# Kernel optimization log

Measured on AMD Instinct MI355X. Metric: run time of the kernel, lower is better.

## Reference

```python
import jax, jax.numpy as jnp
import numpy as np

N_HEAD = 8
HEAD_DIM = 64
DIM = 512
INNER = N_HEAD * HEAD_DIM
ATT_THRESHOLD = 1e-4
SCALE = HEAD_DIM ** -0.5


def setup_inputs() -> dict:
    key = jax.random.key(0)
    ks = jax.random.split(key, 7)
    b, n, dn = 2, 2048, 2048
    fr = jax.random.normal(ks[0], (b, n, DIM), dtype=jnp.float32)
    dt = jax.random.normal(ks[1], (b, dn, DIM), dtype=jnp.float32)
    s = DIM ** -0.5
    Wq = jax.random.normal(ks[2], (DIM, INNER), dtype=jnp.float32) * s
    Wk = jax.random.normal(ks[3], (DIM, INNER), dtype=jnp.float32) * s
    Wv = jax.random.normal(ks[4], (DIM, INNER), dtype=jnp.float32) * s
    Wo = jax.random.normal(ks[5], (INNER, DIM), dtype=jnp.float32) * (INNER ** -0.5)
    bo = jax.random.normal(ks[6], (DIM,), dtype=jnp.float32) * 0.01
    return {"fr": fr, "dt": dt, "Wq": Wq, "Wk": Wk, "Wv": Wv, "Wo": Wo, "bo": bo}


def reference(fr, dt, Wq, Wk, Wv, Wo, bo):
    b, n, _ = fr.shape
    dn = dt.shape[1]
    # projections -> [b, seq, n_head, head_dim]
    q = (fr @ Wq).reshape(b, n, N_HEAD, HEAD_DIM)
    k = (dt @ Wk).reshape(b, dn, N_HEAD, HEAD_DIM)
    v = (dt @ Wv).reshape(b, dn, N_HEAD, HEAD_DIM)
    # full attention matrix [b, h, n, dn]
    scores = jnp.einsum('bihd,bjhd->bhij', q, k) * SCALE
    attn = jax.nn.softmax(scores, axis=-1)
    # torch .clip(t) with one positional arg clamps the MIN: max(attn, t)
    attn = jnp.maximum(attn, ATT_THRESHOLD) - ATT_THRESHOLD
    attn = attn / jnp.sum(attn, axis=-1, keepdims=True)
    out = jnp.einsum('bhij,bjhd->bihd', attn, v).reshape(b, n, INNER)
    return out @ Wo + bo
```

## Files before the change

kernel.cpp:

```cpp
#include <hip/hip_runtime.h>
#include <hip/hip_bf16.h>

#define BB 2
#define SEQ 2048
#define NHEAD 8
#define HD 64
#define ATT_T 1e-4f
#define QSCALE 0.18033688011112042f

typedef short s16x8 __attribute__((ext_vector_type(8)));
typedef float f32x16 __attribute__((ext_vector_type(16)));

#define MFMA32(a, b, c) __builtin_amdgcn_mfma_f32_32x32x16_bf16((a), (b), (c), 0, 0, 0)
#define EXP2(x) __builtin_amdgcn_exp2f(x)
#define SB0() __builtin_amdgcn_sched_barrier(0)
#define WAITVM0() __builtin_amdgcn_s_waitcnt(0x0F70)
#define WAITVM4() __builtin_amdgcn_s_waitcnt(0x0F74)
#define WAITVM8() __builtin_amdgcn_s_waitcnt(0x0F78)

__device__ __forceinline__ unsigned short bfr(float x) {
  __hip_bfloat16 h = __float2bfloat16(x);
  return __builtin_bit_cast(unsigned short, h);
}
__device__ __forceinline__ unsigned int packbf(float a, float b) {
  return (unsigned int)bfr(a) | ((unsigned int)bfr(b) << 16);
}
__device__ __forceinline__ unsigned int permpack(float a, float b) {
  return __builtin_amdgcn_perm(__builtin_bit_cast(unsigned int, b),
                               __builtin_bit_cast(unsigned int, a), 0x07060302u);
}
__device__ __forceinline__ void async16(const void* g, void* l) {
  __builtin_amdgcn_global_load_lds(
      (const __attribute__((address_space(1))) unsigned int*)g,
      (__attribute__((address_space(3))) unsigned int*)l, 16, 0, 0);
}

__global__ __launch_bounds__(256) void convT(const float* __restrict__ w0,
                                             const float* __restrict__ w1,
                                             const float* __restrict__ w2,
                                             const float* __restrict__ w3,
                                             unsigned short* __restrict__ o0,
                                             unsigned short* __restrict__ o1,
                                             unsigned short* __restrict__ o2,
                                             unsigned short* __restrict__ o3) {
  __shared__ float tle[64][65];
  const float* W = blockIdx.z == 0 ? w0 : blockIdx.z == 1 ? w1 : blockIdx.z == 2 ? w2 : w3;
  unsigned short* WT = blockIdx.z == 0 ? o0 : blockIdx.z == 1 ? o1 : blockIdx.z == 2 ? o2 : o3;
  const int r0 = blockIdx.y * 64, c0 = blockIdx.x * 64;
  const int tr = threadIdx.x >> 4;
  const int tc = threadIdx.x & 15;
  #pragma unroll
  for (int i = 0; i < 4; i++) {
    int r = tr + i * 16;
    float4 v = *(const float4*)(W + (size_t)(r0 + r) * 512 + c0 + tc * 4);
    tle[r][tc * 4 + 0] = v.x;
    tle[r][tc * 4 + 1] = v.y;
    tle[r][tc * 4 + 2] = v.z;
    tle[r][tc * 4 + 3] = v.w;
  }
  __syncthreads();
  #pragma unroll
  for (int i = 0; i < 4; i++) {
    int c = tr + i * 16;
    int rr = tc * 4;
    uint2 p;
    p.x = packbf(tle[rr + 0][c], tle[rr + 1][c]);
    p.y = packbf(tle[rr + 2][c], tle[rr + 3][c]);
    *(uint2*)(WT + (size_t)(c0 + c) * 512 + r0 + rr) = p;
  }
}

__global__ __launch_bounds__(256) void gemm_qkv(const float* __restrict__ frF,
                                                const float* __restrict__ dtF,
                                                const unsigned short* __restrict__ WqT,
                                                const unsigned short* __restrict__ WkT,
                                                const unsigned short* __restrict__ WvT,
                                                unsigned short* __restrict__ Qp,
                                                unsigned short* __restrict__ Kp,
                                                unsigned short* __restrict__ VTp) {
  __shared__ __align__(16) unsigned short smem[24576];
  unsigned short* Asm = smem;
  unsigned short* Bsm = smem + 8192;
  const int tid = threadIdx.x, lane = tid & 63, w = tid >> 6;
  const int l31 = lane & 31, lh = lane >> 5;
  const int m0 = blockIdx.y * 64, n0 = blockIdx.x * 128;
  const int z = blockIdx.z;
  const float* A = z == 0 ? frF : dtF;
  const unsigned short* BT = z == 0 ? WqT : (z == 1 ? WkT : WvT);
  unsigned short* OP = z == 0 ? Qp : (z == 1 ? Kp : VTp);
  const float scale = z == 0 ? QSCALE : 1.0f;

  const int arow = tid >> 2, aseg = tid & 3;
  const float* Ap = A + (size_t)(m0 + arow) * 512 + aseg * 16;
  const int aoff = (arow >> 5) * 2048 + aseg * 512 + (arow & 31) * 8;

  auto stageB = [&](int kt, int buf) {
    const int k0 = kt * 64;
    #pragma unroll
    for (int i = 0; i < 4; i++) {
      int r = w * 4 + i, gn = r >> 2, ks = r & 3;
      async16(BT + (size_t)(n0 + gn * 32 + l31) * 512 + k0 + ks * 16 + lh * 8,
              Bsm + buf * 8192 + r * 512);
    }
  };
  auto ldA = [&](int kt, float4* r4) {
    #pragma unroll
    for (int i = 0; i < 4; i++) r4[i] = *(const float4*)(Ap + kt * 64 + i * 4);
  };
  auto wrA = [&](int buf, const float4* r4) {
    uint4 w0v, w1v;
    w0v.x = packbf(r4[0].x, r4[0].y); w0v.y = packbf(r4[0].z, r4[0].w);
    w0v.z = packbf(r4[1].x, r4[1].y); w0v.w = packbf(r4[1].z, r4[1].w);
    w1v.x = packbf(r4[2].x, r4[2].y); w1v.y = packbf(r4[2].z, r4[2].w);
    w1v.z = packbf(r4[3].x, r4[3].y); w1v.w = packbf(r4[3].z, r4[3].w);
    *(uint4*)(Asm + buf * 4096 + aoff) = w0v;
    *(uint4*)(Asm + buf * 4096 + aoff + 256) = w1v;
  };

  f32x16 acc[2];
  #pragma unroll
  for (int j = 0; j < 2; j++)
    #pragma unroll
    for (int r = 0; r < 16; r++) acc[j][r] = 0.f;

  float4 areg[4];
  ldA(0, areg);
  stageB(0, 0);
  wrA(0, areg);
  ldA(1, areg);

  for (int kt = 0; kt < 8; ++kt) {
    __syncthreads();
    if (kt + 1 < 8) {
      const int nb = (kt + 1) & 1;
      stageB(kt + 1, nb);
      wrA(nb, areg);
      if (kt + 2 < 8) ldA(kt + 2, areg);
    }
    const int buf = kt & 1;
    const unsigned short* as = Asm + buf * 4096 + (w & 1) * 2048;
    const unsigned short* bs = Bsm + buf * 8192 + (w >> 1) * 4096;
    #pragma unroll
    for (int ks = 0; ks < 4; ++ks) {
      s16x8 af = *(const s16x8*)(as + ks * 512 + lane * 8);
      s16x8 b0 = *(const s16x8*)(bs + ks * 512 + lane * 8);
      s16x8 b1 = *(const s16x8*)(bs + 2048 + ks * 512 + lane * 8);
      acc[0] = MFMA32(af, b0, acc[0]);
      acc[1] = MFMA32(af, b1, acc[1]);
    }
  }

  const int wm = (w & 1) * 32, wn = (w >> 1) * 64;
  const int bb = m0 >> 11, s0 = m0 & 2047;
  __syncthreads();
  if (z <= 1) {
    #pragma unroll
    for (int j = 0; j < 2; j++)
      #pragma unroll
      for (int r = 0; r < 16; r++) {
        int mm = wm + (r & 3) + 8 * (r >> 2) + 4 * lh;
        int nn = wn + j * 32 + l31;
        smem[mm * 136 + nn] = bfr(acc[j][r] * scale);
      }
    __syncthreads();
    #pragma unroll
    for (int it = 0; it < 4; ++it) {
      int c = tid + it * 256;
      int mm = c >> 4, seg = c & 15;
      uint4 vdat = *(const uint4*)(smem + mm * 136 + seg * 8);
      int n = n0 + seg * 8, h = n >> 6, d = n & 63;
      *(uint4*)(OP + ((size_t)((bb * NHEAD + h) * SEQ + s0 + mm)) * HD + d) = vdat;
    }
  } else {
    #pragma unroll
    for (int j = 0; j < 2; j++)
      #pragma unroll
      for (int r = 0; r < 16; r += 2) {
        int mm = wm + (r & 3) + 8 * (r >> 2) + 4 * lh;
        int nn = wn + j * 32 + l31;
        *(unsigned int*)(smem + nn * 72 + mm) = packbf(acc[j][r], acc[j][r + 1]);
      }
    __syncthreads();
    #pragma unroll
    for (int it = 0; it < 4; ++it) {
      int c = tid + it * 256;
      int nn = c >> 3, seg = c & 7;
      uint4 vdat = *(const uint4*)(smem + nn * 72 + seg * 8);
      int n = n0 + nn, h = n >> 6, d = n & 63;
      *(uint4*)(OP + ((size_t)((bb * NHEAD + h) * HD + d)) * SEQ + s0 + seg * 8) = vdat;
    }
  }
}

__global__ __launch_bounds__(256) void gemm_out(const unsigned short* __restrict__ A,
                                                const unsigned short* __restrict__ BT,
                                                const float* __restrict__ bias,
                                                float* __restrict__ O) {
  __shared__ __align__(16) unsigned short smem[16384];
  unsigned short* Asm = smem;
  unsigned short* Bsm = smem + 8192;
  const int tid = threadIdx.x, lane = tid & 63, w = tid >> 6;
  const int l31 = lane & 31, lh = lane >> 5;
  const int m0 = blockIdx.y * 64, n0 = blockIdx.x * 64;

  auto stage = [&](int kt, int buf) {
    const int k0 = kt * 64;
    #pragma unroll
    for (int i = 0; i < 2; i++) {
      int r = w * 2 + i, g = r >> 2, ks = r & 3;
      async16(A + (size_t)(m0 + g * 32 + l31) * 512 + k0 + ks * 16 + lh * 8,
              Asm + buf * 4096 + r * 512);
      async16(BT + (size_t)(n0 + g * 32 + l31) * 512 + k0 + ks * 16 + lh * 8,
              Bsm + buf * 4096 + r * 512);
    }
  };

  f32x16 acc;
  #pragma unroll
  for (int r = 0; r < 16; r++) acc[r] = 0.f;

  stage(0, 0);
  for (int kt = 0; kt < 8; ++kt) {
    __syncthreads();
    if (kt + 1 < 8) stage(kt + 1, (kt + 1) & 1);
    const int buf = kt & 1;
    const unsigned short* as = Asm + buf * 4096 + (w & 1) * 2048;
    const unsigned short* bs = Bsm + buf * 4096 + (w >> 1) * 2048;
    #pragma unroll
    for (int ks = 0; ks < 4; ++ks) {
      s16x8 af = *(const s16x8*)(as + ks * 512 + lane * 8);
      s16x8 bf = *(const s16x8*)(bs + ks * 512 + lane * 8);
      acc = MFMA32(af, bf, acc);
    }
  }

  const int wm = (w & 1) * 32, wn = (w >> 1) * 32;
  float bv = bias[n0 + wn + l31];
  #pragma unroll
  for (int r = 0; r < 16; r++) {
    int mm = wm + (r & 3) + 8 * (r >> 2) + 4 * lh;
    O[(size_t)(m0 + mm) * 512 + n0 + wn + l31] = acc[r] + bv;
  }
}

__global__ __launch_bounds__(256, 2) void attn_mfma(const unsigned short* __restrict__ Q,
                                                    const unsigned short* __restrict__ K,
                                                    const unsigned short* __restrict__ VT,
                                                    unsigned short* __restrict__ O) {
  __shared__ __align__(16) unsigned short arena[4][8192];
  __shared__ float larr[4][64];
  __shared__ float warr[4][64];

  const int tid = threadIdx.x;
  const int lane = tid & 63;
  const int w = tid >> 6;
  const int l31 = lane & 31, lh = lane >> 5;

  const int bid = blockIdx.x;
  const int g = bid & 7, j = bid >> 3;
  const int bh = g * 2 + (j >> 5);
  const int qt = j & 31;

  const unsigned short* Qh = Q + (size_t)bh * SEQ * HD;
  const unsigned short* Kh = K + (size_t)bh * SEQ * HD;
  const unsigned short* VTh = VT + (size_t)bh * HD * SEQ;

  s16x8 qf[2][4];
  #pragma unroll
  for (int q2 = 0; q2 < 2; q2++)
    #pragma unroll
    for (int t = 0; t < 4; t++)
      qf[q2][t] = *(const s16x8*)(Qh + (size_t)(qt * 64 + q2 * 32 + l31) * HD + 16 * t + 8 * lh);

  unsigned short* kbuf = &arena[w][0];
  unsigned short* vbuf = &arena[w][4096];
  const int kbase = w * 512;

  auto stageK = [&](int c, int slot) {
    const unsigned short* base = Kh + (size_t)(kbase + c * 32 + l31) * HD + lh * 8;
    #pragma unroll
    for (int tt = 0; tt < 4; tt++)
      async16(base + tt * 16, kbuf + slot * 2048 + tt * 512);
  };
  auto stageV = [&](int c, int slot) {
    #pragma unroll
    for (int dh = 0; dh < 2; dh++)
      #pragma unroll
      for (int kc = 0; kc < 2; kc++)
        async16(VTh + (size_t)(dh * 32 + l31) * SEQ + kbase + c * 32 + kc * 16 + lh * 8,
                vbuf + slot * 2048 + (dh * 2 + kc) * 512);
  };

  float lsum[2] = {0.f, 0.f};
  f32x16 scp[2];

  auto accum_l = [&]() {
    #pragma unroll
    for (int q2 = 0; q2 < 2; q2++) {
      float s0 = 0.f, s1 = 0.f, s2 = 0.f, s3 = 0.f;
      #pragma unroll
      for (int r = 0; r < 4; r++) {
        s0 += EXP2(scp[q2][r]);
        s1 += EXP2(scp[q2][4 + r]);
        s2 += EXP2(scp[q2][8 + r]);
        s3 += EXP2(scp[q2][12 + r]);
      }
      lsum[q2] += (s0 + s1) + (s2 + s3);
    }
  };

  stageK(0, 0);
  for (int c = 0; c < 16; ++c) {
    const int slot = c & 1;
    if (c + 1 < 16) stageK(c + 1, slot ^ 1);
    if (c > 0) accum_l();
    if (c + 1 < 16) { WAITVM4(); } else { WAITVM0(); }
    SB0();
    s16x8 kf[4];
    #pragma unroll
    for (int tt = 0; tt < 4; tt++)
      kf[tt] = *(const s16x8*)(kbuf + slot * 2048 + tt * 512 + lane * 8);
    #pragma unroll
    for (int q2 = 0; q2 < 2; q2++) {
      f32x16 sc;
      #pragma unroll
      for (int r = 0; r < 16; r++) sc[r] = 0.f;
      #pragma unroll
      for (int tt = 0; tt < 4; tt++) sc = MFMA32(kf[tt], qf[q2][tt], sc);
      scp[q2] = sc;
    }
  }
  accum_l();
  #pragma unroll
  for (int q2 = 0; q2 < 2; q2++) lsum[q2] += __shfl_xor(lsum[q2], 32);
  if (lh == 0) { larr[w][l31] = lsum[0]; larr[w][32 + l31] = lsum[1]; }
  __syncthreads();
  float tl[2];
  #pragma unroll
  for (int q2 = 0; q2 < 2; q2++)
    tl[q2] = ATT_T * (larr[0][q2 * 32 + l31] + larr[1][q2 * 32 + l31] +
                      larr[2][q2 * 32 + l31] + larr[3][q2 * 32 + l31]);

  f32x16 acc[2][2];
  #pragma unroll
  for (int q2 = 0; q2 < 2; q2++)
    #pragma unroll
    for (int dh = 0; dh < 2; dh++)
      #pragma unroll
      for (int r = 0; r < 16; r++) acc[q2][dh][r] = 0.f;
  float wacc[2] = {0.f, 0.f};
  s16x8 vfp[2][2];

  auto softmax_pv = [&]() {
    s16x8 pf[2][2];
    #pragma unroll
    for (int q2 = 0; q2 < 2; q2++) {
      uint2 quads[4];
      #pragma unroll
      for (int gq = 0; gq < 4; gq++) {
        float u0 = fmaxf(EXP2(scp[q2][4 * gq + 0]) - tl[q2], 0.f);
        float u1 = fmaxf(EXP2(scp[q2][4 * gq + 1]) - tl[q2], 0.f);
        float u2 = fmaxf(EXP2(scp[q2][4 * gq + 2]) - tl[q2], 0.f);
        float u3 = fmaxf(EXP2(scp[q2][4 * gq + 3]) - tl[q2], 0.f);
        wacc[q2] += (u0 + u1) + (u2 + u3);
        quads[gq].x = permpack(u0, u1);
        quads[gq].y = permpack(u2, u3);
      }
      #pragma unroll
      for (int tp = 0; tp < 2; tp++) {
        uint2 ea, eb;
        ea.x = (unsigned)__shfl_xor((int)quads[2 * tp].x, 32);
        ea.y = (unsigned)__shfl_xor((int)quads[2 * tp].y, 32);
        eb.x = (unsigned)__shfl_xor((int)quads[2 * tp + 1].x, 32);
        eb.y = (unsigned)__shfl_xor((int)quads[2 * tp + 1].y, 32);
        uint4 fr;
        if (lh == 0) { fr.x = quads[2 * tp].x; fr.y = quads[2 * tp].y; fr.z = ea.x; fr.w = ea.y; }
        else         { fr.x = eb.x; fr.y = eb.y; fr.z = quads[2 * tp + 1].x; fr.w = quads[2 * tp + 1].y; }
        pf[q2][tp] = __builtin_bit_cast(s16x8, fr);
      }
    }
    #pragma unroll
    for (int q2 = 0; q2 < 2; q2++)
      #pragma unroll
      for (int dh = 0; dh < 2; dh++) {
        acc[q2][dh] = MFMA32(pf[q2][0], vfp[dh][0], acc[q2][dh]);
        acc[q2][dh] = MFMA32(pf[q2][1], vfp[dh][1], acc[q2][dh]);
      }
  };

  stageK(0, 0);
  stageV(0, 0);
  for (int c = 0; c < 16; ++c) {
    const int slot = c & 1;
    if (c + 1 < 16) { stageK(c + 1, slot ^ 1); stageV(c + 1, slot ^ 1); }
    if (c > 0) softmax_pv();
    if (c + 1 < 16) { WAITVM8(); } else { WAITVM0(); }
    SB0();
    s16x8 kf[4];
    #pragma unroll
    for (int tt = 0; tt < 4; tt++)
      kf[tt] = *(const s16x8*)(kbuf + slot * 2048 + tt * 512 + lane * 8);
    #pragma unroll
    for (int dh = 0; dh < 2; dh++)
      #pragma unroll
      for (int kc = 0; kc < 2; kc++)
        vfp[dh][kc] = *(const s16x8*)(vbuf + slot * 2048 + (dh * 2 + kc) * 512 + lane * 8);
    #pragma unroll
    for (int q2 = 0; q2 < 2; q2++) {
      f32x16 sc;
      #pragma unroll
      for (int r = 0; r < 16; r++) sc[r] = 0.f;
      #pragma unroll
      for (int tt = 0; tt < 4; tt++) sc = MFMA32(kf[tt], qf[q2][tt], sc);
      scp[q2] = sc;
    }
  }
  softmax_pv();

  #pragma unroll
  for (int q2 = 0; q2 < 2; q2++) wacc[q2] += __shfl_xor(wacc[q2], 32);
  if (lh == 0) { warr[w][l31] = wacc[0]; warr[w][32 + l31] = wacc[1]; }
  __syncthreads();

  float* plane0 = (float*)&arena[0][0];
  float* plane1 = (float*)&arena[2][0];

  if (w >= 2) {
    float* pl = (w == 2) ? plane0 : plane1;
    #pragma unroll
    for (int q2 = 0; q2 < 2; q2++)
      #pragma unroll
      for (int dh = 0; dh < 2; dh++)
        #pragma unroll
        for (int r = 0; r < 16; r++) {
          int ql = q2 * 32 + (r & 3) + 8 * (r >> 2) + 4 * lh;
          pl[ql * 64 + dh * 32 + l31] = acc[q2][dh][r];
        }
  }
  __syncthreads();
  if (w < 2) {
    float* pl = (w == 0) ? plane0 : plane1;
    #pragma unroll
    for (int q2 = 0; q2 < 2; q2++)
      #pragma unroll
      for (int dh = 0; dh < 2; dh++)
        #pragma unroll
        for (int r = 0; r < 16; r++) {
          int ql = q2 * 32 + (r & 3) + 8 * (r >> 2) + 4 * lh;
          acc[q2][dh][r] += pl[ql * 64 + dh * 32 + l31];
        }
  }
  __syncthreads();
  if (w == 1) {
    #pragma unroll
    for (int q2 = 0; q2 < 2; q2++)
      #pragma unroll
      for (int dh = 0; dh < 2; dh++)
        #pragma unroll
        for (int r = 0; r < 16; r++) {
          int ql = q2 * 32 + (r & 3) + 8 * (r >> 2) + 4 * lh;
          plane0[ql * 64 + dh * 32 + l31] = acc[q2][dh][r];
        }
  }
  __syncthreads();
  unsigned short* otile = &arena[2][0];
  if (w == 0) {
    #pragma unroll
    for (int q2 = 0; q2 < 2; q2++)
      #pragma unroll
      for (int dh = 0; dh < 2; dh++)
        #pragma unroll
        for (int r = 0; r < 16; r++) {
          int ql = q2 * 32 + (r & 3) + 8 * (r >> 2) + 4 * lh;
          float wt = warr[0][ql] + warr[1][ql] + warr[2][ql] + warr[3][ql];
          float v = (acc[q2][dh][r] + plane0[ql * 64 + dh * 32 + l31]) / wt;
          otile[ql * 64 + dh * 32 + l31] = bfr(v);
        }
  }
  __syncthreads();
  const int b = bh >> 3, h = bh & 7;
  #pragma unroll
  for (int it = 0; it < 2; ++it) {
    int c2 = tid + it * 256;
    int mm = c2 >> 3, seg = c2 & 7;
    uint4 vdat = *(const uint4*)(otile + mm * 64 + seg * 8);
    *(uint4*)(O + ((size_t)(b * SEQ + qt * 64 + mm)) * 512 + h * HD + seg * 8) = vdat;
  }
}

extern "C" void kernel_launch(void* const* d_in, const int* in_sizes, int n_in,
                              void* d_out, int out_size, void* d_ws, size_t ws_size,
                              hipStream_t stream) {
  const float* fr = (const float*)d_in[0];
  const float* dt = (const float*)d_in[1];
  const float* Wq = (const float*)d_in[2];
  const float* Wk = (const float*)d_in[3];
  const float* Wv = (const float*)d_in[4];
  const float* Wo = (const float*)d_in[5];
  const float* bo = (const float*)d_in[6];
  float* out = (float*)d_out;

  const size_t planeE = (size_t)BB * SEQ * 512;
  const size_t wE = 512 * 512;
  unsigned short* p = (unsigned short*)d_ws;
  unsigned short* WqT = p; p += wE;
  unsigned short* WkT = p; p += wE;
  unsigned short* WvT = p; p += wE;
  unsigned short* WoT = p; p += wE;
  unsigned short* Qp  = p; p += planeE;
  unsigned short* Kp  = p; p += planeE;
  unsigned short* VTp = p; p += planeE;
  unsigned short* aoB = p; p += planeE;

  convT<<<dim3(8, 8, 4), 256, 0, stream>>>(Wq, Wk, Wv, Wo, WqT, WkT, WvT, WoT);

  gemm_qkv<<<dim3(4, 64, 3), 256, 0, stream>>>(fr, dt, WqT, WkT, WvT, Qp, Kp, VTp);

  attn_mfma<<<BB * NHEAD * 32, 256, 0, stream>>>(Qp, Kp, VTp, aoB);

  gemm_out<<<dim3(8, 64), 256, 0, stream>>>(aoB, WoT, bo, out);
}
```

Measured before the change: 164.3 us.

## Halve attention query tile, load V into registers, use permlane32 swap

The attention kernel now processes 32 query rows per block instead of 64. It launches twice as many blocks, raises the launch-bounds occupancy target from 2 to 4 blocks, and shrinks LDS use accordingly. V tiles are read straight from global memory into registers with a manually unrolled two-stage ping-pong instead of being staged through LDS. The cross-half lane exchange for the P fragments uses permlane32_swap when the builtin is available. The aim is more latency hiding and less LDS pressure, at the cost of reading K and V twice as often per query and doing more per-block reduction overhead.

```diff
diff --git a/kernel.cpp b/kernel.cpp
--- a/kernel.cpp
+++ b/kernel.cpp
@@ -33,6 +33,20 @@
   __builtin_amdgcn_global_load_lds(
       (const __attribute__((address_space(1))) unsigned int*)g,
       (__attribute__((address_space(3))) unsigned int*)l, 16, 0, 0);
+}
+__device__ __forceinline__ void plswap(unsigned a, unsigned b, int lh,
+                                       unsigned& x, unsigned& z) {
+#if __has_builtin(__builtin_amdgcn_permlane32_swap)
+  typedef unsigned uint2v __attribute__((ext_vector_type(2)));
+  uint2v r = __builtin_amdgcn_permlane32_swap(a, b, false, false);
+  x = r[0];
+  z = r[1];
+#else
+  unsigned ea = (unsigned)__shfl_xor((int)a, 32);
+  unsigned eb = (unsigned)__shfl_xor((int)b, 32);
+  x = lh ? eb : a;
+  z = lh ? b : ea;
+#endif
 }
 
 __global__ __launch_bounds__(256) void convT(const float* __restrict__ w0,
@@ -243,13 +257,13 @@
   }
 }
 
-__global__ __launch_bounds__(256, 2) void attn_mfma(const unsigned short* __restrict__ Q,
+__global__ __launch_bounds__(256, 4) void attn_mfma(const unsigned short* __restrict__ Q,
                                                     const unsigned short* __restrict__ K,
                                                     const unsigned short* __restrict__ VT,
                                                     unsigned short* __restrict__ O) {
-  __shared__ __align__(16) unsigned short arena[4][8192];
-  __shared__ float larr[4][64];
-  __shared__ float warr[4][64];
+  __shared__ __align__(16) unsigned short arena[4][4096];
+  __shared__ float larr[4][32];
+  __shared__ float warr[4][32];
 
   const int tid = threadIdx.x;
   const int lane = tid & 63;
@@ -258,22 +272,19 @@
 
   const int bid = blockIdx.x;
   const int g = bid & 7, j = bid >> 3;
-  const int bh = g * 2 + (j >> 5);
-  const int qt = j & 31;
+  const int bh = g * 2 + (j >> 6);
+  const int qt = j & 63;
 
   const unsigned short* Qh = Q + (size_t)bh * SEQ * HD;
   const unsigned short* Kh = K + (size_t)bh * SEQ * HD;
   const unsigned short* VTh = VT + (size_t)bh * HD * SEQ;
 
-  s16x8 qf[2][4];
-  #pragma unroll
-  for (int q2 = 0; q2 < 2; q2++)
-    #pragma unroll
-    for (int t = 0; t < 4; t++)
-      qf[q2][t] = *(const s16x8*)(Qh + (size_t)(qt * 64 + q2 * 32 + l31) * HD + 16 * t + 8 * lh);
+  s16x8 qf[4];
+  #pragma unroll
+  for (int t = 0; t < 4; t++)
+    qf[t] = *(const s16x8*)(Qh + (size_t)(qt * 32 + l31) * HD + 16 * t + 8 * lh);
 
   unsigned short* kbuf = &arena[w][0];
-  unsigned short* vbuf = &arena[w][4096];
   const int kbase = w * 512;
 
   auto stageK = [&](int c, int slot) {
@@ -282,31 +293,32 @@
     for (int tt = 0; tt < 4; tt++)
       async16(base + tt * 16, kbuf + slot * 2048 + tt * 512);
   };
-  auto stageV = [&](int c, int slot) {
-    #pragma unroll
-    for (int dh = 0; dh < 2; dh++)
-      #pragma unroll
-      for (int kc = 0; kc < 2; kc++)
-        async16(VTh + (size_t)(dh * 32 + l31) * SEQ + kbase + c * 32 + kc * 16 + lh * 8,
-                vbuf + slot * 2048 + (dh * 2 + kc) * 512);
-  };
-
-  float lsum[2] = {0.f, 0.f};
-  f32x16 scp[2];
-
+
+  f32x16 scp;
+  auto qkt = [&](int slot) {
+    s16x8 kf[4];
+    #pragma unroll
+    for (int tt = 0; tt < 4; tt++)
+      kf[tt] = *(const s16x8*)(kbuf + slot * 2048 + tt * 512 + lane * 8);
+    f32x16 sc;
+    #pragma unroll
+    for (int r = 0; r < 16; r++) sc[r] = 0.f;
+    #pragma unroll
+    for (int tt = 0; tt < 4; tt++) sc = MFMA32(kf[tt], qf[tt], sc);
+    scp = sc;
+  };
+
+  float lsum = 0.f;
   auto accum_l = [&]() {
-    #pragma unroll
-    for (int q2 = 0; q2 < 2; q2++) {
-      float s0 = 0.f, s1 = 0.f, s2 = 0.f, s3 = 0.f;
-      #pragma unroll
-      for (int r = 0; r < 4; r++) {
-        s0 += EXP2(scp[q2][r]);
-        s1 += EXP2(scp[q2][4 + r]);
-        s2 += EXP2(scp[q2][8 + r]);
-        s3 += EXP2(scp[q2][12 + r]);
-      }
-      lsum[q2] += (s0 + s1) + (s2 + s3);
-    }
+    float s0 = 0.f, s1 = 0.f, s2 = 0.f, s3 = 0.f;
+    #pragma unroll
+    for (int r = 0; r < 4; r++) {
+      s0 += EXP2(scp[r]);
+      s1 += EXP2(scp[4 + r]);
+      s2 += EXP2(scp[8 + r]);
+      s3 += EXP2(scp[12 + r]);
+    }
+    lsum += (s0 + s1) + (s2 + s3);
   };
 
   stageK(0, 0);
@@ -316,175 +328,138 @@
     if (c > 0) accum_l();
     if (c + 1 < 16) { WAITVM4(); } else { WAITVM0(); }
     SB0();
-    s16x8 kf[4];
-    #pragma unroll
-    for (int tt = 0; tt < 4; tt++)
-      kf[tt] = *(const s16x8*)(kbuf + slot * 2048 + tt * 512 + lane * 8);
-    #pragma unroll
-    for (int q2 = 0; q2 < 2; q2++) {
-      f32x16 sc;
-      #pragma unroll
-      for (int r = 0; r < 16; r++) sc[r] = 0.f;
-      #pragma unroll
-      for (int tt = 0; tt < 4; tt++) sc = MFMA32(kf[tt], qf[q2][tt], sc);
-      scp[q2] = sc;
-    }
+    qkt(slot);
   }
   accum_l();
-  #pragma unroll
-  for (int q2 = 0; q2 < 2; q2++) lsum[q2] += __shfl_xor(lsum[q2], 32);
-  if (lh == 0) { larr[w][l31] = lsum[0]; larr[w][32 + l31] = lsum[1]; }
-  __syncthreads();
-  float tl[2];
-  #pragma unroll
-  for (int q2 = 0; q2 < 2; q2++)
-    tl[q2] = ATT_T * (larr[0][q2 * 32 + l31] + larr[1][q2 * 32 + l31] +
-                      larr[2][q2 * 32 + l31] + larr[3][q2 * 32 + l31]);
-
-  f32x16 acc[2][2];
-  #pragma unroll
-  for (int q2 = 0; q2 < 2; q2++)
+  lsum += __shfl_xor(lsum, 32);
+  if (lh == 0) larr[w][l31] = lsum;
+  __syncthreads();
+  const float tl = ATT_T * (larr[0][l31] + larr[1][l31] + larr[2][l31] + larr[3][l31]);
+
+  f32x16 acc[2];
+  #pragma unroll
+  for (int dh = 0; dh < 2; dh++)
+    #pragma unroll
+    for (int r = 0; r < 16; r++) acc[dh][r] = 0.f;
+  float wacc = 0.f;
+  s16x8 vrA[4], vrB[4];
+
+  auto loadV = [&](int c, s16x8(&vr)[4]) {
     #pragma unroll
     for (int dh = 0; dh < 2; dh++)
       #pragma unroll
-      for (int r = 0; r < 16; r++) acc[q2][dh][r] = 0.f;
-  float wacc[2] = {0.f, 0.f};
-  s16x8 vfp[2][2];
-
-  auto softmax_pv = [&]() {
-    s16x8 pf[2][2];
-    #pragma unroll
-    for (int q2 = 0; q2 < 2; q2++) {
-      uint2 quads[4];
-      #pragma unroll
-      for (int gq = 0; gq < 4; gq++) {
-        float u0 = fmaxf(EXP2(scp[q2][4 * gq + 0]) - tl[q2], 0.f);
-        float u1 = fmaxf(EXP2(scp[q2][4 * gq + 1]) - tl[q2], 0.f);
-        float u2 = fmaxf(EXP2(scp[q2][4 * gq + 2]) - tl[q2], 0.f);
-        float u3 = fmaxf(EXP2(scp[q2][4 * gq + 3]) - tl[q2], 0.f);
-        wacc[q2] += (u0 + u1) + (u2 + u3);
-        quads[gq].x = permpack(u0, u1);
-        quads[gq].y = permpack(u2, u3);
-      }
-      #pragma unroll
-      for (int tp = 0; tp < 2; tp++) {
-        uint2 ea, eb;
-        ea.x = (unsigned)__shfl_xor((int)quads[2 * tp].x, 32);
-        ea.y = (unsigned)__shfl_xor((int)quads[2 * tp].y, 32);
-        eb.x = (unsigned)__shfl_xor((int)quads[2 * tp + 1].x, 32);
-        eb.y = (unsigned)__shfl_xor((int)quads[2 * tp + 1].y, 32);
-        uint4 fr;
-        if (lh == 0) { fr.x = quads[2 * tp].x; fr.y = quads[2 * tp].y; fr.z = ea.x; fr.w = ea.y; }
-        else         { fr.x = eb.x; fr.y = eb.y; fr.z = quads[2 * tp + 1].x; fr.w = quads[2 * tp + 1].y; }
-        pf[q2][tp] = __builtin_bit_cast(s16x8, fr);
-      }
-    }
-    #pragma unroll
-    for (int q2 = 0; q2 < 2; q2++)
-      #pragma unroll
-      for (int dh = 0; dh < 2; dh++) {
-        acc[q2][dh] = MFMA32(pf[q2][0], vfp[dh][0], acc[q2][dh]);
-        acc[q2][dh] = MFMA32(pf[q2][1], vfp[dh][1], acc[q2][dh]);
-      }
+      for (int kc = 0; kc < 2; kc++)
+        vr[dh * 2 + kc] = *(const s16x8*)(VTh + (size_t)(dh * 32 + l31) * SEQ +
+                                          kbase + c * 32 + kc * 16 + lh * 8);
+  };
+  auto softmax_pv = [&](const s16x8(&vr)[4]) {
+    uint2 quads[4];
+    #pragma unroll
+    for (int gq = 0; gq < 4; gq++) {
+      float u0 = fmaxf(EXP2(scp[4 * gq + 0]) - tl, 0.f);
+      float u1 = fmaxf(EXP2(scp[4 * gq + 1]) - tl, 0.f);
+      float u2 = fmaxf(EXP2(scp[4 * gq + 2]) - tl, 0.f);
+      float u3 = fmaxf(EXP2(scp[4 * gq + 3]) - tl, 0.f);
+      wacc += (u0 + u1) + (u2 + u3);
+      quads[gq].x = permpack(u0, u1);
+      quads[gq].y = permpack(u2, u3);
+    }
+    s16x8 pf[2];
+    #pragma unroll
+    for (int tp = 0; tp < 2; tp++) {
+      unsigned x0, z0, x1, z1;
+      plswap(quads[2 * tp].x, quads[2 * tp + 1].x, lh, x0, z0);
+      plswap(quads[2 * tp].y, quads[2 * tp + 1].y, lh, x1, z1);
+      uint4 fr;
+      fr.x = x0; fr.y = x1; fr.z = z0; fr.w = z1;
+      pf[tp] = __builtin_bit_cast(s16x8, fr);
+    }
+    #pragma unroll
+    for (int dh = 0; dh < 2; dh++) {
+      acc[dh] = MFMA32(pf[0], vr[dh * 2 + 0], acc[dh]);
+      acc[dh] = MFMA32(pf[1], vr[dh * 2 + 1], acc[dh]);
+    }
   };
 
   stageK(0, 0);
-  stageV(0, 0);
-  for (int c = 0; c < 16; ++c) {
-    const int slot = c & 1;
-    if (c + 1 < 16) { stageK(c + 1, slot ^ 1); stageV(c + 1, slot ^ 1); }
-    if (c > 0) softmax_pv();
-    if (c + 1 < 16) { WAITVM8(); } else { WAITVM0(); }
+  loadV(0, vrA);
+  for (int cc = 0; cc < 16; cc += 2) {
+    if (cc > 0) softmax_pv(vrB);
+    stageK(cc + 1, 1);
+    loadV(cc + 1, vrB);
+    WAITVM8();
     SB0();
-    s16x8 kf[4];
-    #pragma unroll
-    for (int tt = 0; tt < 4; tt++)
-      kf[tt] = *(const s16x8*)(kbuf + slot * 2048 + tt * 512 + lane * 8);
-    #pragma unroll
-    for (int dh = 0; dh < 2; dh++)
-      #pragma unroll
-      for (int kc = 0; kc < 2; kc++)
-        vfp[dh][kc] = *(const s16x8*)(vbuf + slot * 2048 + (dh * 2 + kc) * 512 + lane * 8);
-    #pragma unroll
-    for (int q2 = 0; q2 < 2; q2++) {
-      f32x16 sc;
-      #pragma unroll
-      for (int r = 0; r < 16; r++) sc[r] = 0.f;
-      #pragma unroll
-      for (int tt = 0; tt < 4; tt++) sc = MFMA32(kf[tt], qf[q2][tt], sc);
-      scp[q2] = sc;
-    }
-  }
-  softmax_pv();
-
-  #pragma unroll
-  for (int q2 = 0; q2 < 2; q2++) wacc[q2] += __shfl_xor(wacc[q2], 32);
-  if (lh == 0) { warr[w][l31] = wacc[0]; warr[w][32 + l31] = wacc[1]; }
+    qkt(0);
+    softmax_pv(vrA);
+    if (cc + 2 < 16) {
+      stageK(cc + 2, 0);
+      loadV(cc + 2, vrA);
+      WAITVM8();
+    } else {
+      WAITVM0();
+    }
+    SB0();
+    qkt(1);
+  }
+  softmax_pv(vrB);
+
+  wacc += __shfl_xor(wacc, 32);
+  if (lh == 0) warr[w][l31] = wacc;
   __syncthreads();
 
   float* plane0 = (float*)&arena[0][0];
-  float* plane1 = (float*)&arena[2][0];
+  float* plane1 = (float*)&arena[1][0];
 
   if (w >= 2) {
     float* pl = (w == 2) ? plane0 : plane1;
     #pragma unroll
-    for (int q2 = 0; q2 < 2; q2++)
-      #pragma unroll
-      for (int dh = 0; dh < 2; dh++)
-        #pragma unroll
-        for (int r = 0; r < 16; r++) {
-          int ql = q2 * 32 + (r & 3) + 8 * (r >> 2) + 4 * lh;
-          pl[ql * 64 + dh * 32 + l31] = acc[q2][dh][r];
-        }
+    for (int dh = 0; dh < 2; dh++)
+      #pragma unroll
+      for (int r = 0; r < 16; r++) {
+        int ql = (r & 3) + 8 * (r >> 2) + 4 * lh;
+        pl[ql * 64 + dh * 32 + l31] = acc[dh][r];
+      }
   }
   __syncthreads();
   if (w < 2) {
     float* pl = (w == 0) ? plane0 : plane1;
     #pragma unroll
-    for (int q2 = 0; q2 < 2; q2++)
-      #pragma unroll
-      for (int dh = 0; dh < 2; dh++)
-        #pragma unroll
-        for (int r = 0; r < 16; r++) {
-          int ql = q2 * 32 + (r & 3) + 8 * (r >> 2) + 4 * lh;
-          acc[q2][dh][r] += pl[ql * 64 + dh * 32 + l31];
-        }
+    for (int dh = 0; dh < 2; dh++)
+      #pragma unroll
+      for (int r = 0; r < 16; r++) {
+        int ql = (r & 3) + 8 * (r >> 2) + 4 * lh;
+        acc[dh][r] += pl[ql * 64 + dh * 32 + l31];
+      }
   }
   __syncthreads();
   if (w == 1) {
     #pragma unroll
-    for (int q2 = 0; q2 < 2; q2++)
-      #pragma unroll
-      for (int dh = 0; dh < 2; dh++)
-        #pragma unroll
-        for (int r = 0; r < 16; r++) {
-          int ql = q2 * 32 + (r & 3) + 8 * (r >> 2) + 4 * lh;
-          plane0[ql * 64 + dh * 32 + l31] = acc[q2][dh][r];
-        }
+    for (int dh = 0; dh < 2; dh++)
+      #pragma unroll
+      for (int r = 0; r < 16; r++) {
+        int ql = (r & 3) + 8 * (r >> 2) + 4 * lh;
+        plane0[ql * 64 + dh * 32 + l31] = acc[dh][r];
+      }
   }
   __syncthreads();
   unsigned short* otile = &arena[2][0];
   if (w == 0) {
     #pragma unroll
-    for (int q2 = 0; q2 < 2; q2++)
-      #pragma unroll
-      for (int dh = 0; dh < 2; dh++)
-        #pragma unroll
-        for (int r = 0; r < 16; r++) {
-          int ql = q2 * 32 + (r & 3) + 8 * (r >> 2) + 4 * lh;
-          float wt = warr[0][ql] + warr[1][ql] + warr[2][ql] + warr[3][ql];
-          float v = (acc[q2][dh][r] + plane0[ql * 64 + dh * 32 + l31]) / wt;
-          otile[ql * 64 + dh * 32 + l31] = bfr(v);
-        }
+    for (int dh = 0; dh < 2; dh++)
+      #pragma unroll
+      for (int r = 0; r < 16; r++) {
+        int ql = (r & 3) + 8 * (r >> 2) + 4 * lh;
+        float wt = warr[0][ql] + warr[1][ql] + warr[2][ql] + warr[3][ql];
+        float v = (acc[dh][r] + plane0[ql * 64 + dh * 32 + l31]) / wt;
+        otile[ql * 64 + dh * 32 + l31] = bfr(v);
+      }
   }
   __syncthreads();
   const int b = bh >> 3, h = bh & 7;
-  #pragma unroll
-  for (int it = 0; it < 2; ++it) {
-    int c2 = tid + it * 256;
-    int mm = c2 >> 3, seg = c2 & 7;
+  {
+    int mm = tid >> 3, seg = tid & 7;
     uint4 vdat = *(const uint4*)(otile + mm * 64 + seg * 8);
-    *(uint4*)(O + ((size_t)(b * SEQ + qt * 64 + mm)) * 512 + h * HD + seg * 8) = vdat;
+    *(uint4*)(O + ((size_t)(b * SEQ + qt * 32 + mm)) * 512 + h * HD + seg * 8) = vdat;
   }
 }
 
@@ -516,7 +491,7 @@
 
   gemm_qkv<<<dim3(4, 64, 3), 256, 0, stream>>>(fr, dt, WqT, WkT, WvT, Qp, Kp, VTp);
 
-  attn_mfma<<<BB * NHEAD * 32, 256, 0, stream>>>(Qp, Kp, VTp, aoB);
+  attn_mfma<<<BB * NHEAD * 64, 256, 0, stream>>>(Qp, Kp, VTp, aoB);
 
   gemm_out<<<dim3(8, 64), 256, 0, stream>>>(aoB, WoT, bo, out);
 }
```

After: 225.9 us. 37.5% more time.

## Load V fragments directly into registers and use permlane32 swap for P

Applied to the files above, without the earlier changes.

The second attention pass no longer stages V^T tiles through LDS. Each wave loads its V fragments from global memory straight into double-buffered registers, and the loop is unrolled by two so register buffers A and B alternate with the K LDS slots. This halves the per-wave LDS arena and removes the LDS round trip for V, at the cost of more VGPRs and exposed global latency. The P-fragment exchange across wave halves now uses the permlane32_swap builtin when available, replacing four shuffles and selects per pair.

```diff
diff --git a/kernel.cpp b/kernel.cpp
--- a/kernel.cpp
+++ b/kernel.cpp
@@ -33,6 +33,20 @@
   __builtin_amdgcn_global_load_lds(
       (const __attribute__((address_space(1))) unsigned int*)g,
       (__attribute__((address_space(3))) unsigned int*)l, 16, 0, 0);
+}
+__device__ __forceinline__ void plswap(unsigned a, unsigned b, int lh,
+                                       unsigned& x, unsigned& z) {
+#if __has_builtin(__builtin_amdgcn_permlane32_swap)
+  typedef unsigned uint2v __attribute__((ext_vector_type(2)));
+  uint2v r = __builtin_amdgcn_permlane32_swap(a, b, false, false);
+  x = r[0];
+  z = r[1];
+#else
+  unsigned ea = (unsigned)__shfl_xor((int)a, 32);
+  unsigned eb = (unsigned)__shfl_xor((int)b, 32);
+  x = lh ? eb : a;
+  z = lh ? b : ea;
+#endif
 }
 
 __global__ __launch_bounds__(256) void convT(const float* __restrict__ w0,
@@ -247,7 +261,7 @@
                                                     const unsigned short* __restrict__ K,
                                                     const unsigned short* __restrict__ VT,
                                                     unsigned short* __restrict__ O) {
-  __shared__ __align__(16) unsigned short arena[4][8192];
+  __shared__ __align__(16) unsigned short arena[4][4096];
   __shared__ float larr[4][64];
   __shared__ float warr[4][64];
 
@@ -273,7 +287,6 @@
       qf[q2][t] = *(const s16x8*)(Qh + (size_t)(qt * 64 + q2 * 32 + l31) * HD + 16 * t + 8 * lh);
 
   unsigned short* kbuf = &arena[w][0];
-  unsigned short* vbuf = &arena[w][4096];
   const int kbase = w * 512;
 
   auto stageK = [&](int c, int slot) {
@@ -282,18 +295,25 @@
     for (int tt = 0; tt < 4; tt++)
       async16(base + tt * 16, kbuf + slot * 2048 + tt * 512);
   };
-  auto stageV = [&](int c, int slot) {
-    #pragma unroll
-    for (int dh = 0; dh < 2; dh++)
-      #pragma unroll
-      for (int kc = 0; kc < 2; kc++)
-        async16(VTh + (size_t)(dh * 32 + l31) * SEQ + kbase + c * 32 + kc * 16 + lh * 8,
-                vbuf + slot * 2048 + (dh * 2 + kc) * 512);
+
+  f32x16 scp[2];
+  auto qkt = [&](int slot) {
+    s16x8 kf[4];
+    #pragma unroll
+    for (int tt = 0; tt < 4; tt++)
+      kf[tt] = *(const s16x8*)(kbuf + slot * 2048 + tt * 512 + lane * 8);
+    #pragma unroll
+    for (int q2 = 0; q2 < 2; q2++) {
+      f32x16 sc;
+      #pragma unroll
+      for (int r = 0; r < 16; r++) sc[r] = 0.f;
+      #pragma unroll
+      for (int tt = 0; tt < 4; tt++) sc = MFMA32(kf[tt], qf[q2][tt], sc);
+      scp[q2] = sc;
+    }
   };
 
   float lsum[2] = {0.f, 0.f};
-  f32x16 scp[2];
-
   auto accum_l = [&]() {
     #pragma unroll
     for (int q2 = 0; q2 < 2; q2++) {
@@ -316,19 +336,7 @@
     if (c > 0) accum_l();
     if (c + 1 < 16) { WAITVM4(); } else { WAITVM0(); }
     SB0();
-    s16x8 kf[4];
-    #pragma unroll
-    for (int tt = 0; tt < 4; tt++)
-      kf[tt] = *(const s16x8*)(kbuf + slot * 2048 + tt * 512 + lane * 8);
-    #pragma unroll
-    for (int q2 = 0; q2 < 2; q2++) {
-      f32x16 sc;
-      #pragma unroll
-      for (int r = 0; r < 16; r++) sc[r] = 0.f;
-      #pragma unroll
-      for (int tt = 0; tt < 4; tt++) sc = MFMA32(kf[tt], qf[q2][tt], sc);
-      scp[q2] = sc;
-    }
+    qkt(slot);
   }
   accum_l();
   #pragma unroll
@@ -349,9 +357,17 @@
       #pragma unroll
       for (int r = 0; r < 16; r++) acc[q2][dh][r] = 0.f;
   float wacc[2] = {0.f, 0.f};
-  s16x8 vfp[2][2];
-
-  auto softmax_pv = [&]() {
+  s16x8 vrA[4], vrB[4];
+
+  auto loadV = [&](int c, s16x8(&vr)[4]) {
+    #pragma unroll
+    for (int dh = 0; dh < 2; dh++)
+      #pragma unroll
+      for (int kc = 0; kc < 2; kc++)
+        vr[dh * 2 + kc] = *(const s16x8*)(VTh + (size_t)(dh * 32 + l31) * SEQ +
+                                          kbase + c * 32 + kc * 16 + lh * 8);
+  };
+  auto softmax_pv = [&](const s16x8(&vr)[4]) {
     s16x8 pf[2][2];
     #pragma unroll
     for (int q2 = 0; q2 < 2; q2++) {
@@ -368,14 +384,11 @@
       }
       #pragma unroll
       for (int tp = 0; tp < 2; tp++) {
-        uint2 ea, eb;
-        ea.x = (unsigned)__shfl_xor((int)quads[2 * tp].x, 32);
-        ea.y = (unsigned)__shfl_xor((int)quads[2 * tp].y, 32);
-        eb.x = (unsigned)__shfl_xor((int)quads[2 * tp + 1].x, 32);
-        eb.y = (unsigned)__shfl_xor((int)quads[2 * tp + 1].y, 32);
+        unsigned x0, z0, x1, z1;
+        plswap(quads[2 * tp].x, quads[2 * tp + 1].x, lh, x0, z0);
+        plswap(quads[2 * tp].y, quads[2 * tp + 1].y, lh, x1, z1);
         uint4 fr;
-        if (lh == 0) { fr.x = quads[2 * tp].x; fr.y = quads[2 * tp].y; fr.z = ea.x; fr.w = ea.y; }
-        else         { fr.x = eb.x; fr.y = eb.y; fr.z = quads[2 * tp + 1].x; fr.w = quads[2 * tp + 1].y; }
+        fr.x = x0; fr.y = x1; fr.z = z0; fr.w = z1;
         pf[q2][tp] = __builtin_bit_cast(s16x8, fr);
       }
     }
@@ -383,39 +396,32 @@
     for (int q2 = 0; q2 < 2; q2++)
       #pragma unroll
       for (int dh = 0; dh < 2; dh++) {
-        acc[q2][dh] = MFMA32(pf[q2][0], vfp[dh][0], acc[q2][dh]);
-        acc[q2][dh] = MFMA32(pf[q2][1], vfp[dh][1], acc[q2][dh]);
+        acc[q2][dh] = MFMA32(pf[q2][0], vr[dh * 2 + 0], acc[q2][dh]);
+        acc[q2][dh] = MFMA32(pf[q2][1], vr[dh * 2 + 1], acc[q2][dh]);
       }
   };
 
   stageK(0, 0);
-  stageV(0, 0);
-  for (int c = 0; c < 16; ++c) {
-    const int slot = c & 1;
-    if (c + 1 < 16) { stageK(c + 1, slot ^ 1); stageV(c + 1, slot ^ 1); }
-    if (c > 0) softmax_pv();
-    if (c + 1 < 16) { WAITVM8(); } else { WAITVM0(); }
+  loadV(0, vrA);
+  for (int cc = 0; cc < 16; cc += 2) {
+    if (cc > 0) softmax_pv(vrB);
+    stageK(cc + 1, 1);
+    loadV(cc + 1, vrB);
+    WAITVM8();
     SB0();
-    s16x8 kf[4];
-    #pragma unroll
-    for (int tt = 0; tt < 4; tt++)
-      kf[tt] = *(const s16x8*)(kbuf + slot * 2048 + tt * 512 + lane * 8);
-    #pragma unroll
-    for (int dh = 0; dh < 2; dh++)
-      #pragma unroll
-      for (int kc = 0; kc < 2; kc++)
-        vfp[dh][kc] = *(const s16x8*)(vbuf + slot * 2048 + (dh * 2 + kc) * 512 + lane * 8);
-    #pragma unroll
-    for (int q2 = 0; q2 < 2; q2++) {
-      f32x16 sc;
-      #pragma unroll
-      for (int r = 0; r < 16; r++) sc[r] = 0.f;
-      #pragma unroll
-      for (int tt = 0; tt < 4; tt++) sc = MFMA32(kf[tt], qf[q2][tt], sc);
-      scp[q2] = sc;
-    }
-  }
-  softmax_pv();
+    qkt(0);
+    softmax_pv(vrA);
+    if (cc + 2 < 16) {
+      stageK(cc + 2, 0);
+      loadV(cc + 2, vrA);
+      WAITVM8();
+    } else {
+      WAITVM0();
+    }
+    SB0();
+    qkt(1);
+  }
+  softmax_pv(vrB);
 
   #pragma unroll
   for (int q2 = 0; q2 < 2; q2++) wacc[q2] += __shfl_xor(wacc[q2], 32);
```

After: 162.4 us. Within noise of the previous version (-1.1%).
